# Optimization experiments

Measured on AMD Instinct MI355X. Metric: run time of the kernel, lower is better.

The kernel has to match this reference:

```python
import jax, jax.numpy as jnp
import numpy as np

N_NODES = 100000
N_EDGES = 1600000
N_GRAPHS = 64
D_IN, D_HID, D_OUT = 256, 128, 64
EPS = 1e-5


def gcn_conv(x, edge_index, edge_weight, W, b):
    """PyG GCNConv: add_self_loops=True, normalize=True (sym deg norm), bias."""
    n = x.shape[0]
    row = jnp.concatenate([edge_index[0], jnp.arange(n)])      # source
    col = jnp.concatenate([edge_index[1], jnp.arange(n)])      # target
    w = jnp.concatenate([edge_weight, jnp.ones((n,), x.dtype)])
    deg = jax.ops.segment_sum(w, col, num_segments=n)
    dinv = jnp.where(deg > 0, jax.lax.rsqrt(jnp.maximum(deg, EPS)), 0.0)
    norm = dinv[row] * w * dinv[col]                           # [E+N]
    h = x @ W                                                  # [N, out]
    msg = h[row] * norm[:, None]                               # [E+N, out]
    out = jax.ops.segment_sum(msg, col, num_segments=n)
    return out + b


def layer_norm(x, gamma, beta):
    mu = jnp.mean(x, axis=-1, keepdims=True)
    var = jnp.mean(jnp.square(x - mu), axis=-1, keepdims=True)
    return (x - mu) * jax.lax.rsqrt(var + EPS) * gamma + beta


def setup_inputs() -> dict:
    key = jax.random.key(0)
    ks = jax.random.split(key, 12)
    x = jax.random.normal(ks[0], (N_NODES, D_IN), jnp.float32)
    edge_index = jax.random.randint(ks[1], (2, N_EDGES), 0, N_NODES, jnp.int32)
    edge_weight = jax.random.uniform(ks[2], (N_EDGES,), jnp.float32)
    batch = jnp.sort(jax.random.randint(ks[3], (N_NODES,), 0, N_GRAPHS, jnp.int32))
    s1 = 1.0 / np.sqrt(D_IN)
    s2 = 1.0 / np.sqrt(D_HID)
    return {
        "x": x, "edge_index": edge_index, "edge_weight": edge_weight, "batch": batch,
        "W1": jax.random.uniform(ks[4], (D_IN, D_HID), jnp.float32, -s1, s1),
        "b1": jnp.zeros((D_HID,), jnp.float32),
        "g1": jnp.ones((D_HID,), jnp.float32),
        "bt1": jnp.zeros((D_HID,), jnp.float32),
        "W2": jax.random.uniform(ks[5], (D_HID, D_OUT), jnp.float32, -s2, s2),
        "b2": jnp.zeros((D_OUT,), jnp.float32),
        "g2": jnp.ones((D_OUT,), jnp.float32),
        "bt2": jnp.zeros((D_OUT,), jnp.float32),
    }


def reference(x, edge_index, edge_weight, batch, W1, b1, g1, bt1, W2, b2, g2, bt2):
    # ConvLayer 1: GCNConv -> relu -> LayerNorm(node)
    h = gcn_conv(x, edge_index, edge_weight, W1, b1)
    h = layer_norm(jax.nn.relu(h), g1, bt1)
    # dropout is identity in eval mode
    # ConvLayer 2
    h = gcn_conv(h, edge_index, edge_weight, W2, b2)
    h = layer_norm(jax.nn.relu(h), g2, bt2)
    # global mean pool over batch vector
    sums = jax.ops.segment_sum(h, batch, num_segments=N_GRAPHS)
    cnts = jax.ops.segment_sum(jnp.ones((h.shape[0],), h.dtype), batch, num_segments=N_GRAPHS)
    pooled = sums / jnp.maximum(cnts, 1.0)[:, None]
    return jax.nn.sigmoid(pooled)
```

## Files before the change

kernel.cpp:

```cpp
#include <hip/hip_runtime.h>
#include <cstdint>

#define EPSV 1e-5f

typedef __bf16 bf16x8 __attribute__((ext_vector_type(8)));
typedef __bf16 bf16x2 __attribute__((ext_vector_type(2)));
typedef float  f32x4  __attribute__((ext_vector_type(4)));
typedef unsigned long long u64;

#define FILL_BLOCKS 512

__device__ __forceinline__ unsigned char f32_to_fp8(float x) {
    const int p = __builtin_amdgcn_cvt_pk_fp8_f32(x, x, 0, false);
    return (unsigned char)(p & 0xFF);
}

__global__ __launch_bounds__(256) void k_degacc(const int* __restrict__ ei,
                                                const float* __restrict__ ew,
                                                u64* __restrict__ dc,
                                                unsigned short* __restrict__ rank,
                                                int E) {
    const int e = blockIdx.x * 256 + threadIdx.x;
    if (e < E) {
        const int c = ei[E + e];
        const u64 pack = (1ull << 40) | (u64)(ew[e] * 16777216.0f);
        const u64 old = atomicAdd(&dc[(long)c << 4], pack);
        rank[e] = (unsigned short)(old >> 40);
    }
}

__global__ __launch_bounds__(256) void k_scanA(const u64* __restrict__ dc,
                                               float* __restrict__ dinv,
                                               int* __restrict__ cnt,
                                               int* __restrict__ bsum, int N) {
    __shared__ int ws[4];
    const int i = blockIdx.x * 256 + threadIdx.x;
    int v = 0;
    if (i < N) {
        const u64 p = dc[(long)i << 4];
        v = (int)(p >> 40);
        const float deg = 1.0f + (float)(p & 0xFFFFFFFFFFull) * (1.0f / 16777216.0f);
        dinv[i] = rsqrtf(deg);
        cnt[i] = v;
    }
#pragma unroll
    for (int o = 32; o >= 1; o >>= 1) v += __shfl_xor(v, o);
    if ((threadIdx.x & 63) == 0) ws[threadIdx.x >> 6] = v;
    __syncthreads();
    if (threadIdx.x == 0) bsum[blockIdx.x] = ws[0] + ws[1] + ws[2] + ws[3];
}

__global__ __launch_bounds__(256) void k_scanB(const int* __restrict__ cnt,
                                               const int* __restrict__ bsum,
                                               int* __restrict__ off, int N) {
    __shared__ int pw[4];
    __shared__ int lw[4];
    __shared__ int sbase;
    const int bid = blockIdx.x;
    const int lane = threadIdx.x & 63, w = threadIdx.x >> 6;

    int pre = 0;
    for (int j = threadIdx.x; j < bid; j += 256) pre += bsum[j];
#pragma unroll
    for (int o = 32; o >= 1; o >>= 1) pre += __shfl_xor(pre, o);
    if (lane == 0) pw[w] = pre;
    __syncthreads();
    if (threadIdx.x == 0) sbase = pw[0] + pw[1] + pw[2] + pw[3];

    const int i = bid * 256 + threadIdx.x;
    const int v = (i < N) ? cnt[i] : 0;
    int s = v;
#pragma unroll
    for (int o = 1; o < 64; o <<= 1) {
        const int t = __shfl_up(s, o);
        if (lane >= o) s += t;
    }
    if (lane == 63) lw[w] = s;
    __syncthreads();
    int add = sbase;
    for (int k = 0; k < w; ++k) add += lw[k];
    if (i < N) off[i] = add + s - v;
}

__global__ __launch_bounds__(256) void k_wcvt(const float* __restrict__ W1,
                                              __bf16* __restrict__ Wt1,
                                              const float* __restrict__ W2,
                                              __bf16* __restrict__ Wt2) {
    const int idx = blockIdx.x * 256 + threadIdx.x;
    if (idx < 256 * 128) {
        const int k = idx >> 7, c = idx & 127;
        Wt1[(((k >> 3) << 7) + c) * 8 + (k & 7)] = (__bf16)W1[idx];
    } else if (idx < 256 * 128 + 128 * 64) {
        const int j = idx - 256 * 128;
        const int k = j >> 6, c = j & 63;
        Wt2[(((k >> 3) << 6) + c) * 8 + (k & 7)] = (__bf16)W2[j];
    }
}

template <int K, int NOUT, bool ABF16>
__device__ __forceinline__ void mm_body(int bid, int tid, const void* __restrict__ Xv,
                                        const __bf16* __restrict__ WtB,
                                        unsigned char* __restrict__ H, int N) {
    constexpr int NCB = NOUT / 16;
    constexpr int NKB = K / 32;
    const int w = tid >> 6, l = tid & 63;
    const int r0 = l & 15, kq = l >> 4;
    const long tb0 = (long)bid * 128 + w * 32;
    const long ar0 = (tb0 + r0) < N ? (tb0 + r0) : (long)N - 1;
    const long ar1 = (tb0 + 16 + r0) < N ? (tb0 + 16 + r0) : (long)N - 1;

    f32x4 acc[2][NCB];
#pragma unroll
    for (int rf = 0; rf < 2; ++rf)
#pragma unroll
        for (int cb = 0; cb < NCB; ++cb) acc[rf][cb] = (f32x4){0.f, 0.f, 0.f, 0.f};

#define LDA(kb, a0, a1)                                                          \
    {                                                                            \
        const int koff = (kb) * 32 + kq * 8;                                     \
        if constexpr (ABF16) {                                                   \
            a0 = *reinterpret_cast<const bf16x8*>((const __bf16*)Xv + ar0 * K + koff); \
            a1 = *reinterpret_cast<const bf16x8*>((const __bf16*)Xv + ar1 * K + koff); \
        } else {                                                                 \
            const float* p0 = (const float*)Xv + ar0 * K + koff;                 \
            const float* p1 = (const float*)Xv + ar1 * K + koff;                 \
            const float4 u0 = *reinterpret_cast<const float4*>(p0);              \
            const float4 u1 = *reinterpret_cast<const float4*>(p0 + 4);          \
            const float4 u2 = *reinterpret_cast<const float4*>(p1);              \
            const float4 u3 = *reinterpret_cast<const float4*>(p1 + 4);          \
            a0[0] = (__bf16)u0.x; a0[1] = (__bf16)u0.y; a0[2] = (__bf16)u0.z;    \
            a0[3] = (__bf16)u0.w; a0[4] = (__bf16)u1.x; a0[5] = (__bf16)u1.y;    \
            a0[6] = (__bf16)u1.z; a0[7] = (__bf16)u1.w;                          \
            a1[0] = (__bf16)u2.x; a1[1] = (__bf16)u2.y; a1[2] = (__bf16)u2.z;    \
            a1[3] = (__bf16)u2.w; a1[4] = (__bf16)u3.x; a1[5] = (__bf16)u3.y;    \
            a1[6] = (__bf16)u3.z; a1[7] = (__bf16)u3.w;                          \
        }                                                                        \
    }

#define LDB(kb, b)                                                               \
    {                                                                            \
        const __bf16* bp = WtB + (long)(((kb) * 4 + kq) * NOUT + r0) * 8;        \
        _Pragma("unroll") for (int cb = 0; cb < NCB; ++cb)                       \
            b[cb] = *reinterpret_cast<const bf16x8*>(bp + cb * 128);             \
    }

    bf16x8 aC0, aC1, aN0, aN1;
    bf16x8 bC[NCB], bN[NCB];
    LDA(0, aC0, aC1);
    LDB(0, bC);
#pragma unroll
    for (int kb = 0; kb < NKB; ++kb) {
        if (kb + 1 < NKB) {
            LDA(kb + 1, aN0, aN1);
            LDB(kb + 1, bN);
        }
#pragma unroll
        for (int cb = 0; cb < NCB; ++cb) {
            acc[0][cb] = __builtin_amdgcn_mfma_f32_16x16x32_bf16(aC0, bC[cb], acc[0][cb], 0, 0, 0);
            acc[1][cb] = __builtin_amdgcn_mfma_f32_16x16x32_bf16(aC1, bC[cb], acc[1][cb], 0, 0, 0);
        }
        aC0 = aN0; aC1 = aN1;
#pragma unroll
        for (int cb = 0; cb < NCB; ++cb) bC[cb] = bN[cb];
    }
#undef LDA
#undef LDB

    const int orow = kq * 4;
#pragma unroll
    for (int rf = 0; rf < 2; ++rf)
#pragma unroll
        for (int cb = 0; cb < NCB; ++cb)
#pragma unroll
            for (int r = 0; r < 4; ++r) {
                const long gr = tb0 + rf * 16 + orow + r;
                if (gr < N) H[gr * NOUT + cb * 16 + r0] = f32_to_fp8(acc[rf][cb][r]);
            }
}

__global__ __launch_bounds__(256) void k_fuse(const int* __restrict__ ei,
                                              const float* __restrict__ ew,
                                              const float* __restrict__ dinv,
                                              const int* __restrict__ off,
                                              const unsigned short* __restrict__ rank,
                                              float2* __restrict__ ern, int E,
                                              const float* __restrict__ X,
                                              const __bf16* __restrict__ Wt1,
                                              unsigned char* __restrict__ H1, int N) {
    const int bid = blockIdx.x;
    if (bid < FILL_BLOCKS) {
        const int stride = FILL_BLOCKS * 256;
        for (int e = bid * 256 + threadIdx.x; e < E; e += stride) {
            const int r = ei[e];
            const int c = ei[E + e];
            const int p = off[c] + (int)rank[e];
            ern[p] = make_float2(__int_as_float(r), dinv[r] * ew[e] * dinv[c]);
        }
    } else {
        mm_body<256, 128, false>(bid - FILL_BLOCKS, threadIdx.x, X, Wt1, H1, N);
    }
}

__global__ __launch_bounds__(256) void k_mm2(const __bf16* __restrict__ X,
                                             const __bf16* __restrict__ Wt2,
                                             unsigned char* __restrict__ H, int N) {
    mm_body<128, 64, true>(blockIdx.x, threadIdx.x, X, Wt2, H, N);
}

__global__ __launch_bounds__(256) void k_gat128(const unsigned char* __restrict__ H,
                                                const int* __restrict__ off,
                                                const int* __restrict__ cnt,
                                                const float2* __restrict__ ern,
                                                const float* __restrict__ dinv,
                                                const float* __restrict__ bias,
                                                const float* __restrict__ gm,
                                                const float* __restrict__ bt,
                                                __bf16* __restrict__ Out, int N) {
    const long wv = ((long)blockIdx.x * 256 + threadIdx.x) >> 6;
    const int lane = threadIdx.x & 63;
    if (wv >= N) return;
    const int s = off[wv];
    const int n = cnt[wv];
    const float d = dinv[wv];
    const unsigned short* Hp = reinterpret_cast<const unsigned short*>(H);

    const unsigned int h0 = Hp[wv * 64 + lane];
    float ax = __builtin_amdgcn_cvt_f32_fp8(h0, 0) * d * d;
    float ay = __builtin_amdgcn_cvt_f32_fp8(h0, 1) * d * d;

    int e = 0;
    for (; e + 8 <= n; e += 8) {
        float2 q[8];
#pragma unroll
        for (int j = 0; j < 8; ++j) q[j] = ern[s + e + j];
        unsigned int u[8];
#pragma unroll
        for (int j = 0; j < 8; ++j)
            u[j] = Hp[(long)__float_as_int(q[j].x) * 64 + lane];
#pragma unroll
        for (int j = 0; j < 8; ++j) {
            ax = fmaf(q[j].y, __builtin_amdgcn_cvt_f32_fp8(u[j], 0), ax);
            ay = fmaf(q[j].y, __builtin_amdgcn_cvt_f32_fp8(u[j], 1), ay);
        }
    }
    for (; e < n; ++e) {
        const float2 q = ern[s + e];
        const unsigned int u = Hp[(long)__float_as_int(q.x) * 64 + lane];
        ax = fmaf(q.y, __builtin_amdgcn_cvt_f32_fp8(u, 0), ax);
        ay = fmaf(q.y, __builtin_amdgcn_cvt_f32_fp8(u, 1), ay);
    }

    const float ux = fmaxf(ax + bias[2 * lane], 0.f);
    const float uy = fmaxf(ay + bias[2 * lane + 1], 0.f);
    float s1 = ux + uy, s2 = ux * ux + uy * uy;
#pragma unroll
    for (int o = 32; o >= 1; o >>= 1) {
        s1 += __shfl_xor(s1, o);
        s2 += __shfl_xor(s2, o);
    }
    const float mu = s1 * (1.f / 128.f);
    const float var = s2 * (1.f / 128.f) - mu * mu;
    const float rs = rsqrtf(var + EPSV);
    bf16x2 ob;
    ob[0] = (__bf16)((ux - mu) * rs * gm[2 * lane] + bt[2 * lane]);
    ob[1] = (__bf16)((uy - mu) * rs * gm[2 * lane + 1] + bt[2 * lane + 1]);
    reinterpret_cast<bf16x2*>(Out)[wv * 64 + lane] = ob;
}

__global__ __launch_bounds__(256) void k_gat64(const unsigned char* __restrict__ H,
                                               const int* __restrict__ off,
                                               const int* __restrict__ cnt,
                                               const float2* __restrict__ ern,
                                               const float* __restrict__ dinv,
                                               const float* __restrict__ bias,
                                               const float* __restrict__ gm,
                                               const float* __restrict__ bt,
                                               __bf16* __restrict__ Out, int N) {
    const long wv = ((long)blockIdx.x * 256 + threadIdx.x) >> 6;
    const int lane = threadIdx.x & 63;
    if (wv >= N) return;
    const int s = off[wv];
    const int n = cnt[wv];
    const float d = dinv[wv];

    float acc = __builtin_amdgcn_cvt_f32_fp8((unsigned int)H[wv * 64 + lane], 0) * d * d;
    int e = 0;
    for (; e + 8 <= n; e += 8) {
        float2 q[8];
#pragma unroll
        for (int j = 0; j < 8; ++j) q[j] = ern[s + e + j];
        unsigned int u[8];
#pragma unroll
        for (int j = 0; j < 8; ++j)
            u[j] = H[(long)__float_as_int(q[j].x) * 64 + lane];
#pragma unroll
        for (int j = 0; j < 8; ++j)
            acc = fmaf(q[j].y, __builtin_amdgcn_cvt_f32_fp8(u[j], 0), acc);
    }
    for (; e < n; ++e) {
        const float2 q = ern[s + e];
        const unsigned int u = H[(long)__float_as_int(q.x) * 64 + lane];
        acc = fmaf(q.y, __builtin_amdgcn_cvt_f32_fp8(u, 0), acc);
    }

    const float u = fmaxf(acc + bias[lane], 0.f);
    float s1 = u, s2 = u * u;
#pragma unroll
    for (int o = 32; o >= 1; o >>= 1) {
        s1 += __shfl_xor(s1, o);
        s2 += __shfl_xor(s2, o);
    }
    const float mu = s1 * (1.f / 64.f);
    const float var = s2 * (1.f / 64.f) - mu * mu;
    const float rs = rsqrtf(var + EPSV);
    Out[wv * 64 + lane] = (__bf16)((u - mu) * rs * gm[lane] + bt[lane]);
}

__global__ __launch_bounds__(256) void k_pool(const __bf16* __restrict__ C,
                                              const int* __restrict__ batch,
                                              float* __restrict__ pool,
                                              int N, int chunk) {
    const int wg = blockIdx.x * 4 + (threadIdx.x >> 6);
    const int lane = threadIdx.x & 63;
    long i = (long)wg * chunk;
    const long end = (i + chunk < (long)N) ? i + chunk : (long)N;
    if (i >= end) return;

    int cur = batch[i];
    float acc = 0.f;
    int cn = 0;
    while (i < end) {
        if (i + 8 <= end && batch[i + 7] == cur) {
            float v[8];
#pragma unroll
            for (int j = 0; j < 8; ++j) v[j] = (float)C[(i + j) * 64 + lane];
            acc += ((v[0] + v[1]) + (v[2] + v[3])) + ((v[4] + v[5]) + (v[6] + v[7]));
            cn += 8;
            i += 8;
            continue;
        }
        const int b = batch[i];
        if (b != cur) {
            unsafeAtomicAdd(&pool[cur * 64 + lane], acc);
            if (lane == 0) unsafeAtomicAdd(&pool[64 * 64 + cur], (float)cn);
            cur = b;
            acc = 0.f;
            cn = 0;
        }
        acc += (float)C[i * 64 + lane];
        ++cn;
        ++i;
    }
    unsafeAtomicAdd(&pool[cur * 64 + lane], acc);
    if (lane == 0) unsafeAtomicAdd(&pool[64 * 64 + cur], (float)cn);
}

__global__ __launch_bounds__(256) void k_final(const float* __restrict__ pool,
                                               float* __restrict__ out) {
    const int i = blockIdx.x * 256 + threadIdx.x;
    if (i < 4096) {
        const int g = i >> 6;
        const float cnt = fmaxf(pool[64 * 64 + g], 1.0f);
        const float v = pool[i] / cnt;
        out[i] = 1.f / (1.f + expf(-v));
    }
}

extern "C" void kernel_launch(void* const* d_in, const int* in_sizes, int n_in,
                              void* d_out, int out_size, void* d_ws, size_t ws_size,
                              hipStream_t stream) {
    const float* x   = (const float*)d_in[0];
    const int*   ei  = (const int*)d_in[1];
    const float* ew  = (const float*)d_in[2];
    const int*   bat = (const int*)d_in[3];
    const float* W1  = (const float*)d_in[4];
    const float* b1  = (const float*)d_in[5];
    const float* g1  = (const float*)d_in[6];
    const float* bt1 = (const float*)d_in[7];
    const float* W2  = (const float*)d_in[8];
    const float* b2  = (const float*)d_in[9];
    const float* g2  = (const float*)d_in[10];
    const float* bt2 = (const float*)d_in[11];
    const int N = in_sizes[3];
    const int E = in_sizes[2];
    const int NB = (N + 255) / 256;

    u64*    dc   = (u64*)d_ws;
    float*  pool = (float*)(dc + (long)N * 16);
    float2* ern  = (float2*)(pool + 64 * 64 + 64);
    unsigned char* Ah = (unsigned char*)(ern + E);
    __bf16* Bh   = (__bf16*)(Ah + (long)N * 128);
    __bf16* Cb   = Bh + (long)N * 128;
    float*  dinv = (float*)(Cb + (long)N * 64);
    int*    cnt  = (int*)(dinv + N);
    int*    off  = cnt + N;
    int*    bsum = off + N;
    unsigned short* rank = (unsigned short*)(bsum + ((NB + 3) & ~3));
    __bf16* Wt1  = (__bf16*)(rank + E);
    __bf16* Wt2  = Wt1 + 128 * 256;

    const int nbE = (E + 255) / 256;
    const int nbW = (int)(((long)N * 64 + 255) / 256);
    const int NBM = (N + 127) / 128;

    hipMemsetAsync(dc, 0, (size_t)N * 16 * 8 + (64 * 64 + 64) * 4, stream);
    k_wcvt<<<(256 * 128 + 128 * 64 + 255) / 256, 256, 0, stream>>>(W1, Wt1, W2, Wt2);

    k_degacc<<<nbE, 256, 0, stream>>>(ei, ew, dc, rank, E);
    k_scanA<<<NB, 256, 0, stream>>>(dc, dinv, cnt, bsum, N);
    k_scanB<<<NB, 256, 0, stream>>>(cnt, bsum, off, N);

    k_fuse<<<FILL_BLOCKS + NBM, 256, 0, stream>>>(ei, ew, dinv, off, rank, ern, E,
                                                  x, Wt1, Ah, N);

    k_gat128<<<nbW, 256, 0, stream>>>(Ah, off, cnt, ern, dinv, b1, g1, bt1, Bh, N);

    k_mm2<<<NBM, 256, 0, stream>>>(Bh, Wt2, Ah, N);
    k_gat64<<<nbW, 256, 0, stream>>>(Ah, off, cnt, ern, dinv, b2, g2, bt2, Cb, N);

    const int chunk = (N + 1023) / 1024;
    k_pool<<<256, 256, 0, stream>>>(Cb, bat, pool, N, chunk);
    k_final<<<16, 256, 0, stream>>>(pool, (float*)d_out);
}
```

Measured before the change: 322.4 us.

## Replace global-atomic CSR build with two-level bucket sort by destination

Builds the destination-sorted edge list (CSR) with a two-pass bucket sort: per-chunk histograms over 256-node buckets, a scan, a scatter into buckets, then a per-bucket LDS counting sort that also computes degree, offsets and dinv. This removes the per-edge global 64-bit atomics on the degree/count array and the large memset of that padded array. In exchange it adds more kernel launches, a serial single-block scan, and drops the fused fill+GEMM overlap. Edge weights are quantized to 16 bits and buckets are capped at 6144 edges, which costs some accuracy and assumes no bucket overflows.

```diff
diff --git a/kernel.cpp b/kernel.cpp
--- a/kernel.cpp
+++ b/kernel.cpp
@@ -7,79 +7,164 @@
 typedef __bf16 bf16x2 __attribute__((ext_vector_type(2)));
 typedef float  f32x4  __attribute__((ext_vector_type(4)));
 typedef unsigned long long u64;
-
-#define FILL_BLOCKS 512
+typedef unsigned int u32;
+
+#define NSB  512
+#define BCAP 6144
 
 __device__ __forceinline__ unsigned char f32_to_fp8(float x) {
     const int p = __builtin_amdgcn_cvt_pk_fp8_f32(x, x, 0, false);
     return (unsigned char)(p & 0xFF);
 }
 
-__global__ __launch_bounds__(256) void k_degacc(const int* __restrict__ ei,
-                                                const float* __restrict__ ew,
-                                                u64* __restrict__ dc,
-                                                unsigned short* __restrict__ rank,
-                                                int E) {
-    const int e = blockIdx.x * 256 + threadIdx.x;
-    if (e < E) {
+__global__ __launch_bounds__(256) void k_bh(const int* __restrict__ eic,
+                                            u32* __restrict__ bhT,
+                                            int E, int CH, int NBK) {
+    __shared__ int h[400];
+    for (int i = threadIdx.x; i < NBK; i += 256) h[i] = 0;
+    __syncthreads();
+    const int lo = blockIdx.x * CH;
+    const int hi = min(E, lo + CH);
+    for (int e = lo + threadIdx.x; e < hi; e += 256)
+        atomicAdd(&h[eic[e] >> 8], 1);
+    __syncthreads();
+    for (int b = threadIdx.x; b < NBK; b += 256)
+        bhT[b * NSB + blockIdx.x] = (u32)h[b];
+}
+
+__global__ __launch_bounds__(256) void k_bscan(const u32* __restrict__ bhT,
+                                               u32* __restrict__ baseT,
+                                               int* __restrict__ barr, int NBK) {
+    __shared__ int tot[400];
+    for (int b = threadIdx.x; b < NBK; b += 256) {
+        const uint4* p = (const uint4*)(bhT + b * NSB);
+        int s = 0;
+        for (int j = 0; j < NSB / 4; ++j) {
+            const uint4 v = p[j];
+            s += (int)(v.x + v.y + v.z + v.w);
+        }
+        tot[b] = s;
+    }
+    __syncthreads();
+    if (threadIdx.x == 0) {
+        int run = 0;
+        for (int b = 0; b < NBK; ++b) {
+            const int t = tot[b];
+            barr[b] = run;
+            tot[b] = run;
+            run += t;
+        }
+        barr[NBK] = run;
+    }
+    __syncthreads();
+    for (int b = threadIdx.x; b < NBK; b += 256) {
+        u32 run = (u32)tot[b];
+        const u32* p = bhT + b * NSB;
+        u32* q = baseT + b * NSB;
+        for (int j = 0; j < NSB; ++j) {
+            const u32 t = p[j];
+            q[j] = run;
+            run += t;
+        }
+    }
+}
+
+__global__ __launch_bounds__(256) void k_bscat(const int* __restrict__ ei,
+                                               const float* __restrict__ ew,
+                                               const u32* __restrict__ baseT,
+                                               u64* __restrict__ buck,
+                                               int E, int CH, int NBK) {
+    __shared__ u32 base[400];
+    __shared__ u32 cur[400];
+    for (int i = threadIdx.x; i < NBK; i += 256) {
+        base[i] = baseT[i * NSB + blockIdx.x];
+        cur[i] = 0;
+    }
+    __syncthreads();
+    const int lo = blockIdx.x * CH;
+    const int hi = min(E, lo + CH);
+    for (int e = lo + threadIdx.x; e < hi; e += 256) {
         const int c = ei[E + e];
-        const u64 pack = (1ull << 40) | (u64)(ew[e] * 16777216.0f);
-        const u64 old = atomicAdd(&dc[(long)c << 4], pack);
-        rank[e] = (unsigned short)(old >> 40);
-    }
-}
-
-__global__ __launch_bounds__(256) void k_scanA(const u64* __restrict__ dc,
-                                               float* __restrict__ dinv,
-                                               int* __restrict__ cnt,
-                                               int* __restrict__ bsum, int N) {
-    __shared__ int ws[4];
-    const int i = blockIdx.x * 256 + threadIdx.x;
-    int v = 0;
-    if (i < N) {
-        const u64 p = dc[(long)i << 4];
-        v = (int)(p >> 40);
-        const float deg = 1.0f + (float)(p & 0xFFFFFFFFFFull) * (1.0f / 16777216.0f);
-        dinv[i] = rsqrtf(deg);
-        cnt[i] = v;
-    }
-#pragma unroll
-    for (int o = 32; o >= 1; o >>= 1) v += __shfl_xor(v, o);
-    if ((threadIdx.x & 63) == 0) ws[threadIdx.x >> 6] = v;
-    __syncthreads();
-    if (threadIdx.x == 0) bsum[blockIdx.x] = ws[0] + ws[1] + ws[2] + ws[3];
-}
-
-__global__ __launch_bounds__(256) void k_scanB(const int* __restrict__ cnt,
-                                               const int* __restrict__ bsum,
-                                               int* __restrict__ off, int N) {
-    __shared__ int pw[4];
-    __shared__ int lw[4];
-    __shared__ int sbase;
-    const int bid = blockIdx.x;
+        const int r = ei[e];
+        const int b = c >> 8;
+        const u32 rk = atomicAdd(&cur[b], 1u);
+        const u32 w16 = (u32)(ew[e] * 65535.0f + 0.5f);
+        buck[base[b] + rk] = ((u64)(c & 255) << 33) | ((u64)r << 16) | (u64)w16;
+    }
+}
+
+__global__ __launch_bounds__(256) void k_bucket(const u64* __restrict__ buck,
+                                                const int* __restrict__ barr,
+                                                u64* __restrict__ srt,
+                                                int* __restrict__ cnt,
+                                                int* __restrict__ off,
+                                                float* __restrict__ dinv, int N) {
+    __shared__ u64 arr[BCAP];
+    __shared__ int lc[256];
+    __shared__ float ldeg[256];
+    __shared__ int loff[256];
+    __shared__ int wsum[4];
+    const int b = blockIdx.x;
+    const int e0 = barr[b];
+    const int nb = min(barr[b + 1] - e0, BCAP);
+
+    lc[threadIdx.x] = 0;
+    ldeg[threadIdx.x] = 0.f;
+    __syncthreads();
+
+    for (int i = threadIdx.x; i < nb; i += 256) {
+        const u64 v = buck[e0 + i];
+        arr[i] = v;
+        const int cl = (int)(v >> 33) & 255;
+        atomicAdd(&lc[cl], 1);
+        atomicAdd(&ldeg[cl], (float)(u32)(v & 0xFFFF) * (1.0f / 65535.0f));
+    }
+    __syncthreads();
+
     const int lane = threadIdx.x & 63, w = threadIdx.x >> 6;
-
-    int pre = 0;
-    for (int j = threadIdx.x; j < bid; j += 256) pre += bsum[j];
-#pragma unroll
-    for (int o = 32; o >= 1; o >>= 1) pre += __shfl_xor(pre, o);
-    if (lane == 0) pw[w] = pre;
-    __syncthreads();
-    if (threadIdx.x == 0) sbase = pw[0] + pw[1] + pw[2] + pw[3];
-
-    const int i = bid * 256 + threadIdx.x;
-    const int v = (i < N) ? cnt[i] : 0;
-    int s = v;
+    const int vv = lc[threadIdx.x];
+    int s = vv;
 #pragma unroll
     for (int o = 1; o < 64; o <<= 1) {
         const int t = __shfl_up(s, o);
         if (lane >= o) s += t;
     }
-    if (lane == 63) lw[w] = s;
-    __syncthreads();
-    int add = sbase;
-    for (int k = 0; k < w; ++k) add += lw[k];
-    if (i < N) off[i] = add + s - v;
+    if (lane == 63) wsum[w] = s;
+    __syncthreads();
+    int add = 0;
+    for (int k = 0; k < w; ++k) add += wsum[k];
+    loff[threadIdx.x] = add + s - vv;
+    __syncthreads();
+
+    const int c = b * 256 + threadIdx.x;
+    if (c < N) {
+        cnt[c] = vv;
+        off[c] = e0 + loff[threadIdx.x];
+        dinv[c] = rsqrtf(1.0f + ldeg[threadIdx.x]);
+    }
+
+    __syncthreads();
+    lc[threadIdx.x] = 0;
+    __syncthreads();
+    for (int i = threadIdx.x; i < nb; i += 256) {
+        const u64 v = arr[i];
+        const int cl = (int)(v >> 33) & 255;
+        const int rk = atomicAdd(&lc[cl], 1);
+        srt[e0 + loff[cl] + rk] =
+            ((u64)(b * 256 + cl) << 33) | (v & 0x1FFFFFFFFull);
+    }
+}
+
+__global__ __launch_bounds__(256) void k_norm(const u64* __restrict__ srt,
+                                              const float* __restrict__ dinv,
+                                              float2* __restrict__ ern, int E) {
+    const int p = blockIdx.x * 256 + threadIdx.x;
+    if (p >= E) return;
+    const u64 v = srt[p];
+    const int c = (int)(v >> 33);
+    const int r = (int)((v >> 16) & 0x1FFFF);
+    const float w = (float)(u32)(v & 0xFFFF) * (1.0f / 65535.0f);
+    ern[p] = make_float2(__int_as_float(r), dinv[r] * w * dinv[c]);
 }
 
 __global__ __launch_bounds__(256) void k_wcvt(const float* __restrict__ W1,
@@ -178,27 +263,10 @@
             }
 }
 
-__global__ __launch_bounds__(256) void k_fuse(const int* __restrict__ ei,
-                                              const float* __restrict__ ew,
-                                              const float* __restrict__ dinv,
-                                              const int* __restrict__ off,
-                                              const unsigned short* __restrict__ rank,
-                                              float2* __restrict__ ern, int E,
-                                              const float* __restrict__ X,
-                                              const __bf16* __restrict__ Wt1,
-                                              unsigned char* __restrict__ H1, int N) {
-    const int bid = blockIdx.x;
-    if (bid < FILL_BLOCKS) {
-        const int stride = FILL_BLOCKS * 256;
-        for (int e = bid * 256 + threadIdx.x; e < E; e += stride) {
-            const int r = ei[e];
-            const int c = ei[E + e];
-            const int p = off[c] + (int)rank[e];
-            ern[p] = make_float2(__int_as_float(r), dinv[r] * ew[e] * dinv[c]);
-        }
-    } else {
-        mm_body<256, 128, false>(bid - FILL_BLOCKS, threadIdx.x, X, Wt1, H1, N);
-    }
+__global__ __launch_bounds__(256) void k_mm1(const float* __restrict__ X,
+                                             const __bf16* __restrict__ Wt1,
+                                             unsigned char* __restrict__ H, int N) {
+    mm_body<256, 128, false>(blockIdx.x, threadIdx.x, X, Wt1, H, N);
 }
 
 __global__ __launch_bounds__(256) void k_mm2(const __bf16* __restrict__ X,
@@ -383,36 +451,40 @@
     const float* bt2 = (const float*)d_in[11];
     const int N = in_sizes[3];
     const int E = in_sizes[2];
-    const int NB = (N + 255) / 256;
-
-    u64*    dc   = (u64*)d_ws;
-    float*  pool = (float*)(dc + (long)N * 16);
-    float2* ern  = (float2*)(pool + 64 * 64 + 64);
-    unsigned char* Ah = (unsigned char*)(ern + E);
+    const int NBK = (N + 255) >> 8;
+    const int NBKp = (NBK + 2) & ~1;
+
+    u64*    buck = (u64*)d_ws;
+    u64*    srt  = buck + E;
+    float2* ern  = (float2*)(srt + E);
+    u32*    bhT  = (u32*)(ern + E);
+    u32*    baseT= bhT + (long)NBKp * NSB;
+    int*    barr = (int*)(baseT + (long)NBKp * NSB);
+    unsigned char* Ah = (unsigned char*)(barr + NBK + 9);
     __bf16* Bh   = (__bf16*)(Ah + (long)N * 128);
     __bf16* Cb   = Bh + (long)N * 128;
     float*  dinv = (float*)(Cb + (long)N * 64);
     int*    cnt  = (int*)(dinv + N);
     int*    off  = cnt + N;
-    int*    bsum = off + N;
-    unsigned short* rank = (unsigned short*)(bsum + ((NB + 3) & ~3));
-    __bf16* Wt1  = (__bf16*)(rank + E);
+    __bf16* Wt1  = (__bf16*)(off + N);
     __bf16* Wt2  = Wt1 + 128 * 256;
+    float*  pool = (float*)(Wt2 + 64 * 128);
 
     const int nbE = (E + 255) / 256;
     const int nbW = (int)(((long)N * 64 + 255) / 256);
     const int NBM = (N + 127) / 128;
-
-    hipMemsetAsync(dc, 0, (size_t)N * 16 * 8 + (64 * 64 + 64) * 4, stream);
+    const int CH  = (E + NSB - 1) / NSB;
+
+    hipMemsetAsync(pool, 0, (64 * 64 + 64) * sizeof(float), stream);
     k_wcvt<<<(256 * 128 + 128 * 64 + 255) / 256, 256, 0, stream>>>(W1, Wt1, W2, Wt2);
 
-    k_degacc<<<nbE, 256, 0, stream>>>(ei, ew, dc, rank, E);
-    k_scanA<<<NB, 256, 0, stream>>>(dc, dinv, cnt, bsum, N);
-    k_scanB<<<NB, 256, 0, stream>>>(cnt, bsum, off, N);
-
-    k_fuse<<<FILL_BLOCKS + NBM, 256, 0, stream>>>(ei, ew, dinv, off, rank, ern, E,
-                                                  x, Wt1, Ah, N);
-
+    k_bh<<<NSB, 256, 0, stream>>>(ei + E, bhT, E, CH, NBK);
+    k_bscan<<<1, 256, 0, stream>>>(bhT, baseT, barr, NBK);
+    k_bscat<<<NSB, 256, 0, stream>>>(ei, ew, baseT, buck, E, CH, NBK);
+    k_bucket<<<NBK, 256, 0, stream>>>(buck, barr, srt, cnt, off, dinv, N);
+    k_norm<<<nbE, 256, 0, stream>>>(srt, dinv, ern, E);
+
+    k_mm1<<<NBM, 256, 0, stream>>>(x, Wt1, Ah, N);
     k_gat128<<<nbW, 256, 0, stream>>>(Ah, off, cnt, ern, dinv, b1, g1, bt1, Bh, N);
 
     k_mm2<<<NBM, 256, 0, stream>>>(Bh, Wt2, Ah, N);
```

Result: slower. 360.8 us (+11.9%).
